# Kernel tuning notes

Measured on AMD Instinct MI355X. Metric: run time of the kernel, lower is better.

Reference implementation:

```python
import jax, jax.numpy as jnp
import numpy as np

U, D_IN, RANK, N = 128, 10240, 320, 32

def setup_inputs() -> dict:
    key = jax.random.key(0)
    ks = jax.random.split(key, 9)
    s = 0.02
    return {
        "x": jax.random.normal(ks[0], (U, D_IN), jnp.float32),
        "h": jax.random.normal(ks[1], (U, D_IN, N), jnp.float32),
        "W_delta": jax.random.normal(ks[2], (D_IN, RANK), jnp.float32) * s,
        "W_dt": jax.random.normal(ks[3], (RANK, D_IN), jnp.float32) * s,
        "b_dt": jax.random.normal(ks[4], (D_IN,), jnp.float32) * s,
        "W_B": jax.random.normal(ks[5], (D_IN, N), jnp.float32) * s,
        "W_C": jax.random.normal(ks[6], (D_IN, N), jnp.float32) * s,
        # A = -exp(A_log): strictly negative, so exp(delta*A) in (0,1)
        "A": -jnp.exp(jax.random.normal(ks[7], (D_IN, N), jnp.float32) * 0.5),
        "D": jax.random.normal(ks[8], (D_IN,), jnp.float32),
    }

def reference(x, h, W_delta, W_dt, b_dt, W_B, W_C, A, D):
    # dt projection: low-rank then up-proj + bias, softplus (beta=1, threshold=20)
    delta = jax.nn.softplus(x @ W_delta @ W_dt + b_dt)          # [U, D_IN]
    # B and C input-dependent projections
    B = x @ W_B                                                  # [U, N]
    C = x @ W_C                                                  # [U, N]
    # discretize: abar = exp(delta * A); bbar*x = delta * B * x
    abar = jnp.exp(delta[:, :, None] * A[None, :, :])            # [U, D_IN, N]
    bx = (delta * x)[:, :, None] * B[:, None, :]                 # [U, D_IN, N]
    h_new = abar * h + bx                                        # state update
    # output: y_d = sum_n h[d,n] * C[n] + D_d * x_d
    y = jnp.einsum('udn,un->ud', h_new, C) + D[None, :] * x      # [U, D_IN]
    return y, h_new
```

## Files before the change

### kernel.cpp

```cpp
#include <hip/hip_runtime.h>

#define U_    128
#define DIN   10240
#define RANK  320
#define NS    32
#define NTOT  384

__global__ __launch_bounds__(256) void transpose_kernel(
    const float* __restrict__ x, float* __restrict__ xT)
{
    __shared__ float tile[32][33];
    int kb = blockIdx.x * 32, ub = blockIdx.y * 32;
    int tx = threadIdx.x, ty = threadIdx.y;
#pragma unroll
    for (int i = 0; i < 32; i += 8)
        tile[ty + i][tx] = x[(size_t)(ub + ty + i) * DIN + kb + tx];
    __syncthreads();
#pragma unroll
    for (int i = 0; i < 32; i += 8)
        xT[(size_t)(kb + ty + i) * U_ + ub + tx] = tile[tx][ty + i];
}

template<int KCC>
__global__ __launch_bounds__(256) void gemmA_kernel(
    const float* __restrict__ xT,
    const float* __restrict__ Wd, const float* __restrict__ Wb,
    const float* __restrict__ Wc,
    float* __restrict__ partial)
{
    constexpr int KCH   = DIN / KCC;
    constexpr int KHALF = KCH / 2;
    __shared__ float Wl[KCH][32];

    int b  = blockIdx.x;
    int nt = b / KCC;
    int kc = b % KCC;
    int n0 = nt * 32;
    int k0 = kc * KCH;

    const float* W; int ldw, c0;
    if (nt < 10)       { W = Wd; ldw = RANK; c0 = n0; }
    else if (nt == 10) { W = Wb; ldw = NS;   c0 = 0;  }
    else               { W = Wc; ldw = NS;   c0 = 0;  }

    for (int i4 = threadIdx.x; i4 < KCH * 8; i4 += 256) {
        int r = i4 >> 3;
        int c = (i4 & 7) * 4;
        *(float4*)&Wl[r][c] =
            *(const float4*)&W[(size_t)(k0 + r) * ldw + c0 + c];
    }
    __syncthreads();

    int u    = threadIdx.x & 127;
    int half = threadIdx.x >> 7;

    float acc[32];
#pragma unroll
    for (int j = 0; j < 32; ++j) acc[j] = 0.f;

    const float* xp = xT + (size_t)(k0 + half * KHALF) * U_ + u;
    int kbase = half * KHALF;

#pragma unroll 8
    for (int k = 0; k < KHALF; ++k) {
        float xv = xp[(size_t)k * U_];
        const float4* wr = (const float4*)&Wl[kbase + k][0];
#pragma unroll
        for (int j4 = 0; j4 < 8; ++j4) {
            float4 w = wr[j4];
            acc[j4 * 4 + 0] += xv * w.x;
            acc[j4 * 4 + 1] += xv * w.y;
            acc[j4 * 4 + 2] += xv * w.z;
            acc[j4 * 4 + 3] += xv * w.w;
        }
    }

    __syncthreads();
    float* comb = &Wl[0][0];
    if (half == 1) {
#pragma unroll
        for (int j = 0; j < 32; ++j) comb[j * 128 + u] = acc[j];
    }
    __syncthreads();
    if (half == 0) {
        float* out = partial + (size_t)kc * (NTOT * U_) + (size_t)n0 * U_ + u;
#pragma unroll
        for (int j = 0; j < 32; ++j)
            out[(size_t)j * U_] = acc[j] + comb[j * 128 + u];
    }
}

template<int KCC>
__global__ __launch_bounds__(256) void reduce_kernel(
    const float* __restrict__ partial, float* __restrict__ tT,
    float* __restrict__ Bc, float* __restrict__ Cc)
{
    int e = blockIdx.x * 256 + threadIdx.x;
    float s = 0.f;
#pragma unroll 8
    for (int kc = 0; kc < KCC; ++kc)
        s += partial[(size_t)kc * (NTOT * U_) + e];
    int n = e >> 7, u = e & 127;
    if (n < RANK)            tT[e] = s;
    else if (n < RANK + NS)  Bc[u * NS + (n - RANK)] = s;
    else                     Cc[u * NS + (n - RANK - NS)] = s;
}

__global__ __launch_bounds__(128) void delta_kernel(
    const float* __restrict__ tT, const float* __restrict__ Wdt,
    const float* __restrict__ b_dt, float* __restrict__ delta)
{
    __shared__ float ts[RANK][8];
    int b   = blockIdx.x;
    int dt_ = b % 80, ut = b / 80;
    int d   = dt_ * 128 + threadIdx.x;
    int u0  = ut * 8;

    for (int i4 = threadIdx.x; i4 < RANK * 2; i4 += 128) {
        int r = i4 >> 1, c = (i4 & 1) * 4;
        *(float4*)&ts[r][c] = *(const float4*)&tT[(size_t)r * U_ + u0 + c];
    }
    __syncthreads();

    float bias = b_dt[d];
    float acc[8];
#pragma unroll
    for (int i = 0; i < 8; ++i) acc[i] = bias;

#pragma unroll 4
    for (int r = 0; r < RANK; ++r) {
        float w = Wdt[(size_t)r * DIN + d];
        const float4* tp = (const float4*)&ts[r][0];
        float4 t0 = tp[0], t1 = tp[1];
        acc[0] += w * t0.x; acc[1] += w * t0.y;
        acc[2] += w * t0.z; acc[3] += w * t0.w;
        acc[4] += w * t1.x; acc[5] += w * t1.y;
        acc[6] += w * t1.z; acc[7] += w * t1.w;
    }
#pragma unroll
    for (int i = 0; i < 8; ++i) {
        float z = acc[i];
        float sp = (z > 20.f) ? z : log1pf(__expf(z));
        delta[(size_t)(u0 + i) * DIN + d] = sp;
    }
}

__global__ __launch_bounds__(256) void ssm_kernel(
    const float* __restrict__ x, const float* __restrict__ h,
    const float* __restrict__ delta,
    const float* __restrict__ Bc, const float* __restrict__ Cc,
    const float* __restrict__ A, const float* __restrict__ Dvec,
    float* __restrict__ y, float* __restrict__ hnew)
{
    int idx4 = blockIdx.x * 256 + threadIdx.x;
    int n4 = idx4 & 7;
    int ud = idx4 >> 3;
    int d = ud % DIN;
    int u = ud / DIN;

    float dlt = delta[ud];
    float xv  = x[ud];

    float4 hv = ((const float4*)h)[idx4];
    float4 av = ((const float4*)A)[(size_t)d * 8 + n4];
    float4 bv = ((const float4*)Bc)[u * 8 + n4];
    float4 cv = ((const float4*)Cc)[u * 8 + n4];

    float dx = dlt * xv;
    float4 hn;
    hn.x = __expf(dlt * av.x) * hv.x + dx * bv.x;
    hn.y = __expf(dlt * av.y) * hv.y + dx * bv.y;
    hn.z = __expf(dlt * av.z) * hv.z + dx * bv.z;
    hn.w = __expf(dlt * av.w) * hv.w + dx * bv.w;

    ((float4*)hnew)[idx4] = hn;

    float p = hn.x * cv.x + hn.y * cv.y + hn.z * cv.z + hn.w * cv.w;
    p += __shfl_xor(p, 4, 8);
    p += __shfl_xor(p, 2, 8);
    p += __shfl_xor(p, 1, 8);
    if (n4 == 0)
        y[ud] = p + Dvec[d] * xv;
}

extern "C" void kernel_launch(void* const* d_in, const int* in_sizes, int n_in,
                              void* d_out, int out_size, void* d_ws, size_t ws_size,
                              hipStream_t stream)
{
    const float* x   = (const float*)d_in[0];
    const float* h   = (const float*)d_in[1];
    const float* Wd  = (const float*)d_in[2];
    const float* Wdt = (const float*)d_in[3];
    const float* bdt = (const float*)d_in[4];
    const float* Wb  = (const float*)d_in[5];
    const float* Wc  = (const float*)d_in[6];
    const float* A   = (const float*)d_in[7];
    const float* Dv  = (const float*)d_in[8];

    const bool big = ws_size >= (size_t)4505600 * 4;
    const size_t partial_elems = (size_t)(big ? 64 : 32) * NTOT * U_;

    float* ws      = (float*)d_ws;
    float* xT      = ws;
    float* partial = ws + 1310720;
    float* delta   = partial;
    float* tT      = partial + partial_elems;
    float* Bc      = tT + 40960;
    float* Cc      = Bc + 4096;

    float* y    = (float*)d_out;
    float* hnew = y + (size_t)U_ * DIN;

    dim3 tb(32, 8);
    transpose_kernel<<<dim3(DIN / 32, U_ / 32), tb, 0, stream>>>(x, xT);
    if (big) {
        gemmA_kernel<64><<<12 * 64, 256, 0, stream>>>(xT, Wd, Wb, Wc, partial);
        reduce_kernel<64><<<192, 256, 0, stream>>>(partial, tT, Bc, Cc);
    } else {
        gemmA_kernel<32><<<12 * 32, 256, 0, stream>>>(xT, Wd, Wb, Wc, partial);
        reduce_kernel<32><<<192, 256, 0, stream>>>(partial, tT, Bc, Cc);
    }
    delta_kernel<<<80 * 16, 128, 0, stream>>>(tT, Wdt, bdt, delta);
    ssm_kernel  <<<40960, 256, 0, stream>>>(x, h, delta, Bc, Cc, A, Dv, y, hnew);
}
```

Measured before the change: 391.6 us.

## Fuse delta projection with SSM state update in one kernel

Merges the delta GEMV/softplus kernel with the SSM update kernel. Each block computes delta for 8 users × 128 channels, stages delta, delta*x and D*x in shared memory, then streams the matching h and A slices to produce hnew and y. This removes the delta round trip through global memory and one launch. In exchange, the memory-bound state update now runs on only 1280 blocks of 128 threads, which reduces parallelism and latency hiding.

Measured after the change: 403.9 us. 1.03x slower.

```diff
diff --git a/kernel.cpp b/kernel.cpp
--- a/kernel.cpp
+++ b/kernel.cpp
@@ -106,17 +106,27 @@
     else                     Cc[u * NS + (n - RANK - NS)] = s;
 }
 
-__global__ __launch_bounds__(128) void delta_kernel(
+__global__ __launch_bounds__(128) void delta_ssm_kernel(
     const float* __restrict__ tT, const float* __restrict__ Wdt,
-    const float* __restrict__ b_dt, float* __restrict__ delta)
+    const float* __restrict__ b_dt, const float* __restrict__ x,
+    const float* __restrict__ h, const float* __restrict__ A,
+    const float* __restrict__ Bc, const float* __restrict__ Cc,
+    const float* __restrict__ Dvec,
+    float* __restrict__ y, float* __restrict__ hnew)
 {
     __shared__ float ts[RANK][8];
+    __shared__ float dls[8][128];
+    __shared__ float dxs[8][128];
+    __shared__ float Dxs[8][128];
+
+    int tid = threadIdx.x;
     int b   = blockIdx.x;
     int dt_ = b % 80, ut = b / 80;
-    int d   = dt_ * 128 + threadIdx.x;
+    int d0  = dt_ * 128;
+    int d   = d0 + tid;
     int u0  = ut * 8;
 
-    for (int i4 = threadIdx.x; i4 < RANK * 2; i4 += 128) {
+    for (int i4 = tid; i4 < RANK * 2; i4 += 128) {
         int r = i4 >> 1, c = (i4 & 1) * 4;
         *(float4*)&ts[r][c] = *(const float4*)&tT[(size_t)r * U_ + u0 + c];
     }
@@ -137,50 +147,54 @@
         acc[4] += w * t1.x; acc[5] += w * t1.y;
         acc[6] += w * t1.z; acc[7] += w * t1.w;
     }
+
+    float Dv_ = Dvec[d];
 #pragma unroll
     for (int i = 0; i < 8; ++i) {
-        float z = acc[i];
+        float z  = acc[i];
         float sp = (z > 20.f) ? z : log1pf(__expf(z));
-        delta[(size_t)(u0 + i) * DIN + d] = sp;
-    }
-}
-
-__global__ __launch_bounds__(256) void ssm_kernel(
-    const float* __restrict__ x, const float* __restrict__ h,
-    const float* __restrict__ delta,
-    const float* __restrict__ Bc, const float* __restrict__ Cc,
-    const float* __restrict__ A, const float* __restrict__ Dvec,
-    float* __restrict__ y, float* __restrict__ hnew)
-{
-    int idx4 = blockIdx.x * 256 + threadIdx.x;
-    int n4 = idx4 & 7;
-    int ud = idx4 >> 3;
-    int d = ud % DIN;
-    int u = ud / DIN;
-
-    float dlt = delta[ud];
-    float xv  = x[ud];
-
-    float4 hv = ((const float4*)h)[idx4];
-    float4 av = ((const float4*)A)[(size_t)d * 8 + n4];
-    float4 bv = ((const float4*)Bc)[u * 8 + n4];
-    float4 cv = ((const float4*)Cc)[u * 8 + n4];
-
-    float dx = dlt * xv;
-    float4 hn;
-    hn.x = __expf(dlt * av.x) * hv.x + dx * bv.x;
-    hn.y = __expf(dlt * av.y) * hv.y + dx * bv.y;
-    hn.z = __expf(dlt * av.z) * hv.z + dx * bv.z;
-    hn.w = __expf(dlt * av.w) * hv.w + dx * bv.w;
-
-    ((float4*)hnew)[idx4] = hn;
-
-    float p = hn.x * cv.x + hn.y * cv.y + hn.z * cv.z + hn.w * cv.w;
-    p += __shfl_xor(p, 4, 8);
-    p += __shfl_xor(p, 2, 8);
-    p += __shfl_xor(p, 1, 8);
-    if (n4 == 0)
-        y[ud] = p + Dvec[d] * xv;
+        float xv = x[(size_t)(u0 + i) * DIN + d];
+        dls[i][tid] = sp;
+        dxs[i][tid] = sp * xv;
+        Dxs[i][tid] = Dv_ * xv;
+    }
+    __syncthreads();
+
+    int n4  = tid & 7;
+    int dl0 = tid >> 3;
+    const float4* h4 = (const float4*)h;
+    const float4* A4 = (const float4*)A;
+    float4*      hn4 = (float4*)hnew;
+
+    for (int ul = 0; ul < 8; ++ul) {
+        size_t base = ((size_t)(u0 + ul) * DIN + d0) * 8;
+        float4 bv = ((const float4*)Bc)[(u0 + ul) * 8 + n4];
+        float4 cv = ((const float4*)Cc)[(u0 + ul) * 8 + n4];
+#pragma unroll
+        for (int f2 = 0; f2 < 8; ++f2) {
+            int dloc = f2 * 16 + dl0;
+            size_t gi = base + (size_t)dloc * 8 + n4;
+            float4 hv = h4[gi];
+            float4 av = A4[(size_t)(d0 + dloc) * 8 + n4];
+            float dlt = dls[ul][dloc];
+            float dx  = dxs[ul][dloc];
+
+            float4 hn;
+            hn.x = __expf(dlt * av.x) * hv.x + dx * bv.x;
+            hn.y = __expf(dlt * av.y) * hv.y + dx * bv.y;
+            hn.z = __expf(dlt * av.z) * hv.z + dx * bv.z;
+            hn.w = __expf(dlt * av.w) * hv.w + dx * bv.w;
+
+            hn4[gi] = hn;
+
+            float p = hn.x * cv.x + hn.y * cv.y + hn.z * cv.z + hn.w * cv.w;
+            p += __shfl_xor(p, 4, 8);
+            p += __shfl_xor(p, 2, 8);
+            p += __shfl_xor(p, 1, 8);
+            if (n4 == 0)
+                y[(size_t)(u0 + ul) * DIN + d0 + dloc] = p + Dxs[ul][dloc];
+        }
+    }
 }
 
 extern "C" void kernel_launch(void* const* d_in, const int* in_sizes, int n_in,
@@ -203,7 +217,6 @@
     float* ws      = (float*)d_ws;
     float* xT      = ws;
     float* partial = ws + 1310720;
-    float* delta   = partial;
     float* tT      = partial + partial_elems;
     float* Bc      = tT + 40960;
     float* Cc      = Bc + 4096;
@@ -220,6 +233,6 @@
         gemmA_kernel<32><<<12 * 32, 256, 0, stream>>>(xT, Wd, Wb, Wc, partial);
         reduce_kernel<32><<<192, 256, 0, stream>>>(partial, tT, Bc, Cc);
     }
-    delta_kernel<<<80 * 16, 128, 0, stream>>>(tT, Wdt, bdt, delta);
-    ssm_kernel  <<<40960, 256, 0, stream>>>(x, h, delta, Bc, Cc, A, Dv, y, hnew);
-}
+    delta_ssm_kernel<<<1280, 128, 0, stream>>>(tT, Wdt, bdt, x, h, A,
+                                               Bc, Cc, Dv, y, hnew);
+}
```
